# Kernel tuning notes

Measured on AMD Instinct MI355X. Metric: run time of the kernel, lower is better.

The kernel has to match this reference:

```python
import jax, jax.numpy as jnp
import numpy as np
from jax import lax

CR = 16        # opt.cr (temporal dim)
HEADS = 4      # num_heads
DIM = 64       # dim == channel count c
B = 2          # true batch; input batch = B*CR
H = W = 128


def setup_inputs() -> dict:
    key = jax.random.key(0)
    k1, k2, k3, k4 = jax.random.split(key, 4)
    return {
        "x": jax.random.normal(k1, (B * CR, DIM, H, W), jnp.float32),
        "ln_weight": jnp.ones((DIM,), jnp.float32),
        "ln_bias": jnp.zeros((DIM,), jnp.float32),
        "qkv_w": jax.random.normal(k2, (3 * CR, CR), jnp.float32) * 0.05,   # 1x1 conv
        "dw_w": jax.random.normal(k3, (3 * CR, 1, 3, 3), jnp.float32) * 0.1,  # depthwise 3x3
        "proj_w": jax.random.normal(k4, (DIM, DIM), jnp.float32) * 0.05,   # 1x1 conv
        "temperature": jnp.ones((HEADS, 1, 1), jnp.float32),
    }


def reference(x, ln_weight, ln_bias, qkv_w, dw_w, proj_w, temperature):
    b, c, h, w = x.shape
    Bt = b // CR
    # WithBias LayerNorm over channel dim (per spatial location), eps=1e-5
    mu = jnp.mean(x, axis=1, keepdims=True)
    var = jnp.mean(jnp.square(x - mu), axis=1, keepdims=True)
    xn = (x - mu) / jnp.sqrt(var + 1e-5)
    xn = xn * ln_weight[None, :, None, None] + ln_bias[None, :, None, None]
    # (B*cr, c, h, w) -> (B, cr, c, h, w) -> (B*c, cr, h, w)
    x_in = xn.reshape(Bt, CR, c, h, w).transpose(0, 2, 1, 3, 4).reshape(Bt * c, CR, h, w)
    # 1x1 qkv conv (no bias)
    qkv = jnp.einsum('oc,bchw->bohw', qkv_w, x_in)
    # depthwise 3x3 conv, padding 1
    qkv = lax.conv_general_dilated(qkv, dw_w, (1, 1), 'SAME',
                                   feature_group_count=3 * CR,
                                   dimension_numbers=('NCHW', 'OIHW', 'NCHW'))
    q, k, v = jnp.split(qkv, 3, axis=1)
    ch = CR // HEADS  # per-head channel dim

    def heads(t):
        return t.reshape(Bt * c, HEADS, ch, h * w)

    def l2n(t):
        n = jnp.sqrt(jnp.sum(jnp.square(t), axis=-1, keepdims=True))
        return t / jnp.maximum(n, 1e-12)

    q, k, v = heads(q), heads(k), heads(v)
    q, k = l2n(q), l2n(k)
    # transposed (channel) attention: small ch x ch scores
    attn = jnp.einsum('bhcn,bhdn->bhcd', q, k) * temperature[None]
    attn = jax.nn.softmax(attn, axis=-1)
    out = jnp.einsum('bhcd,bhdn->bhcn', attn, v)  # (B*c, heads, ch, hw)
    # (B*c, cr, h, w) -> (B, c, cr, h, w) -> (B*cr, c, h, w)
    out = out.reshape(Bt * c, CR, h, w).reshape(Bt, c, CR, h, w)
    out = out.transpose(0, 2, 1, 3, 4).reshape(b, c, h, w)
    # 1x1 project_out
    return jnp.einsum('oc,bchw->bohw', proj_w, out)
```

## Files before the change

kernel.cpp:

```cpp
#include <hip/hip_runtime.h>
#include <hip/hip_fp16.h>

typedef _Float16 half8_t __attribute__((ext_vector_type(8)));
typedef float float4_t __attribute__((ext_vector_type(4)));

__device__ __forceinline__ float2 h2f2(unsigned int u) {
  return __half22float2(__builtin_bit_cast(__half2, u));
}
__device__ __forceinline__ unsigned int f2h2(float a, float b) {
  return __builtin_bit_cast(unsigned int, __floats2half2_rn(a, b));
}

#if __has_builtin(__builtin_amdgcn_fdot2)
typedef _Float16 h2v __attribute__((ext_vector_type(2)));
__device__ __forceinline__ float fdot2(unsigned int a, unsigned int b, float c) {
  return __builtin_amdgcn_fdot2(__builtin_bit_cast(h2v, a),
                                __builtin_bit_cast(h2v, b), c, false);
}
#else
__device__ __forceinline__ float fdot2(unsigned int a, unsigned int b, float c) {
  float2 fa = h2f2(a), fb = h2f2(b);
  return fmaf(fa.y, fb.y, fmaf(fa.x, fb.x, c));
}
#endif

__global__ __launch_bounds__(256) void k_stats(const float2* __restrict__ x2,
                                               float4* __restrict__ stats4) {
  int id = blockIdx.x * 256 + threadIdx.x;
  int bb = id >> 13;
  int jp = id & 8191;
  const float2* xp = x2 + ((size_t)bb << 19) + jp;
  float s0 = 0.f, q0 = 0.f, s1 = 0.f, q1 = 0.f;
#pragma unroll
  for (int ci = 0; ci < 64; ++ci) {
    float2 v = xp[(size_t)ci << 13];
    s0 += v.x; q0 = fmaf(v.x, v.x, q0);
    s1 += v.y; q1 = fmaf(v.y, v.y, q1);
  }
  float mu0 = s0 * (1.f / 64.f), mu1 = s1 * (1.f / 64.f);
  float4 r;
  r.x = mu0; r.y = rsqrtf(fmaf(-mu0, mu0, q0 * (1.f / 64.f)) + 1e-5f);
  r.z = mu1; r.w = rsqrtf(fmaf(-mu1, mu1, q1 * (1.f / 64.f)) + 1e-5f);
  stats4[id] = r;
}

__global__ __launch_bounds__(256) void k_wpack(
    const float* __restrict__ qkvw, const float* __restrict__ dww,
    const float* __restrict__ projw, unsigned int* __restrict__ qkvpk,
    unsigned int* __restrict__ dwpk, unsigned int* __restrict__ projpk) {
  int t = blockIdx.x * 256 + threadIdx.x;
  if (t < 2048) {
    int o = t >> 5, c2 = t & 31;
    projpk[t] = f2h2(projw[(o << 6) + 2 * c2], projw[(o << 6) + 2 * c2 + 1]);
  } else if (t < 2432) {
    int i = t - 2048;
    int ch = i >> 3, tp = i & 7;
    qkvpk[i] = f2h2(qkvw[(ch << 4) + 2 * tp], qkvw[(ch << 4) + 2 * tp + 1]);
  } else if (t < 2648) {
    int i = t - 2432;
    int pl = i / 9, k = i - pl * 9;
    dwpk[i] = f2h2(dww[18 * pl + k], dww[18 * pl + 9 + k]);
  }
}

__global__ __launch_bounds__(256) void k_fused(
    const float* __restrict__ x, const float2* __restrict__ stats2,
    const float* __restrict__ lnw, const float* __restrict__ lnb,
    const unsigned int* __restrict__ qkvpk, const unsigned int* __restrict__ dwpk,
    unsigned int* __restrict__ vbuf, float* __restrict__ Sacc,
    float* __restrict__ Nacc) {
  __shared__ unsigned int xnl[2944];
  __shared__ unsigned int pre[2976];
  __shared__ unsigned int qk[2080];
  int tid = threadIdx.x;
  int bc = blockIdx.y, bt = bc >> 6, ci = bc & 63;
  int tx0 = (blockIdx.x & 3) << 5;
  int ty0 = (blockIdx.x >> 2) << 3;
  float lw = lnw[ci], lb = lnb[ci];

  {
    size_t xci = ((size_t)(bt * 1024 + ci)) << 14;
    int sb = bt << 18;
#pragma unroll
    for (int it = 0; it < 2; ++it) {
      int pos = tid + (it << 8);
      if (pos < 360) {
        int hy = pos / 36, hx = pos - hy * 36;
        int gy = ty0 + hy - 1, gx = tx0 + hx - 1;
        bool ok = (hx < 34) && ((unsigned)gy < 128u) && ((unsigned)gx < 128u);
        int gp = (gy << 7) + gx;
        unsigned int w[8];
#pragma unroll
        for (int tp = 0; tp < 8; ++tp) {
          unsigned int ww = 0;
          if (ok) {
            float x0 = x[xci + ((size_t)(2 * tp) << 20) + gp];
            float x1 = x[xci + ((size_t)(2 * tp + 1) << 20) + gp];
            float2 s0 = stats2[sb + ((2 * tp) << 14) + gp];
            float2 s1 = stats2[sb + ((2 * tp + 1) << 14) + gp];
            ww = f2h2(fmaf((x0 - s0.x) * s0.y, lw, lb),
                      fmaf((x1 - s1.x) * s1.y, lw, lb));
          }
          w[tp] = ww;
        }
        *reinterpret_cast<uint4*>(&xnl[pos * 4]) = make_uint4(w[0], w[1], w[2], w[3]);
        *reinterpret_cast<uint4*>(&xnl[1472 + pos * 4]) =
            make_uint4(w[4], w[5], w[6], w[7]);
      }
    }
  }
  __syncthreads();

  int lane15 = tid & 15;
  int kg = (tid >> 4) & 3;
  int wv = tid >> 6;
  int jx = tid & 7, iy = (tid >> 3) & 7, pq = wv;

  for (int m = 0; m < 3; ++m) {
    if (m > 0) {
      int pm = m - 1;
      {
        int combo = tid >> 3, pc = tid & 7;
        int hp_ = combo >> 4, cd = combo & 15, cc = cd >> 2, dd = cd & 3;
        const unsigned int* qrow = qk + (4 * hp_ + cc) * 130;
        const unsigned int* krow = qk + (8 + 4 * hp_ + dd) * 130;
        float s = 0.f;
#pragma unroll
        for (int i = 0; i < 8; ++i) {
          uint2 q2 = *reinterpret_cast<const uint2*>(&qrow[2 * pc + (i << 4)]);
          uint2 k2 = *reinterpret_cast<const uint2*>(&krow[2 * pc + (i << 4)]);
          s = fdot2(q2.x, k2.x, s);
          s = fdot2(q2.y, k2.y, s);
        }
        s += __shfl_xor(s, 1); s += __shfl_xor(s, 2); s += __shfl_xor(s, 4);
        if (pc == 0)
          atomicAdd(&Sacc[((bc << 2) + 2 * pm + hp_) * 16 + cc * 4 + dd], s);
      }
      {
        int row = tid >> 4, pc = tid & 15;
        const unsigned int* rp = qk + row * 130;
        float n = 0.f;
#pragma unroll
        for (int i = 0; i < 4; ++i) {
          uint2 v2 = *reinterpret_cast<const uint2*>(&rp[2 * pc + (i << 5)]);
          n = fdot2(v2.x, v2.x, n);
          n = fdot2(v2.y, v2.y, n);
        }
        n += __shfl_xor(n, 1); n += __shfl_xor(n, 2);
        n += __shfl_xor(n, 4); n += __shfl_xor(n, 8);
        if (pc == 0) {
          int g = (row < 8) ? (8 * pm + row) : (16 + 8 * pm + (row - 8));
          atomicAdd(&Nacc[(bc << 5) + g], n);
        }
      }
    }
    {
      int gch = (m < 2)
                    ? ((lane15 < 8) ? (8 * m + lane15) : (16 + 8 * m + (lane15 - 8)))
                    : (32 + lane15);
      uint4 aw = make_uint4(0, 0, 0, 0);
      if (kg < 2) aw = *reinterpret_cast<const uint4*>(&qkvpk[gch * 8 + 4 * kg]);
      half8_t af = __builtin_bit_cast(half8_t, aw);
      float4_t zz = {0.f, 0.f, 0.f, 0.f};
      for (int T = wv; T < 23; T += 4) {
        int hp = T * 16 + lane15;
        uint4 bw = make_uint4(0, 0, 0, 0);
        if (kg < 2)
          bw = *reinterpret_cast<const uint4*>(&xnl[kg * 1472 + hp * 4]);
        half8_t bf = __builtin_bit_cast(half8_t, bw);
        float4_t d = __builtin_amdgcn_mfma_f32_16x16x32_f16(af, bf, zz, 0, 0, 0);
        pre[(2 * kg) * 372 + hp] = f2h2(d[0], d[1]);
        pre[(2 * kg + 1) * 372 + hp] = f2h2(d[2], d[3]);
      }
    }
    __syncthreads();
#pragma unroll
    for (int p2 = 0; p2 < 2; ++p2) {
      int pl = pq + 4 * p2;
      int gpl = (m < 2) ? ((pl < 4) ? (4 * m + pl) : (8 + 4 * m + (pl - 4)))
                        : (16 + pl);
      const unsigned int* wp = dwpk + gpl * 9;
      __half2 a0 = __floats2half2_rn(0.f, 0.f), a1 = a0, a2 = a0, a3 = a0;
      int base = pl * 372 + iy * 36 + 4 * jx;
#pragma unroll
      for (int dy = 0; dy < 3; ++dy) {
        uint4 C0 = *reinterpret_cast<const uint4*>(&pre[base + dy * 36]);
        uint2 C1 = *reinterpret_cast<const uint2*>(&pre[base + dy * 36 + 4]);
        __half2 c0 = __builtin_bit_cast(__half2, C0.x);
        __half2 c1 = __builtin_bit_cast(__half2, C0.y);
        __half2 c2 = __builtin_bit_cast(__half2, C0.z);
        __half2 c3 = __builtin_bit_cast(__half2, C0.w);
        __half2 c4 = __builtin_bit_cast(__half2, C1.x);
        __half2 c5 = __builtin_bit_cast(__half2, C1.y);
        __half2 w0 = __builtin_bit_cast(__half2, wp[dy * 3 + 0]);
        __half2 w1 = __builtin_bit_cast(__half2, wp[dy * 3 + 1]);
        __half2 w2 = __builtin_bit_cast(__half2, wp[dy * 3 + 2]);
        a0 = __hfma2(w0, c0, a0); a0 = __hfma2(w1, c1, a0); a0 = __hfma2(w2, c2, a0);
        a1 = __hfma2(w0, c1, a1); a1 = __hfma2(w1, c2, a1); a1 = __hfma2(w2, c3, a1);
        a2 = __hfma2(w0, c2, a2); a2 = __hfma2(w1, c3, a2); a2 = __hfma2(w2, c4, a2);
        a3 = __hfma2(w0, c3, a3); a3 = __hfma2(w1, c4, a3); a3 = __hfma2(w2, c5, a3);
      }
      unsigned int u0 = __builtin_bit_cast(unsigned int, a0);
      unsigned int u1 = __builtin_bit_cast(unsigned int, a1);
      unsigned int u2 = __builtin_bit_cast(unsigned int, a2);
      unsigned int u3 = __builtin_bit_cast(unsigned int, a3);
      if (m < 2) {
        uint2 E, O;
        E.x = (u0 & 0xFFFFu) | (u1 << 16);
        E.y = (u2 & 0xFFFFu) | (u3 << 16);
        O.x = (u0 >> 16) | (u1 & 0xFFFF0000u);
        O.y = (u2 >> 16) | (u3 & 0xFFFF0000u);
        int pp = iy * 16 + 2 * jx;
        *reinterpret_cast<uint2*>(&qk[(2 * pl) * 130 + pp]) = E;
        *reinterpret_cast<uint2*>(&qk[(2 * pl + 1) * 130 + pp]) = O;
      } else {
        size_t idx = ((size_t)(bc * 8 + pl) << 14) +
                     (size_t)((ty0 + iy) << 7) + tx0 + 4 * jx;
        *reinterpret_cast<uint4*>(&vbuf[idx]) = make_uint4(u0, u1, u2, u3);
      }
    }
    if (m < 2) __syncthreads();
  }
}

__global__ __launch_bounds__(256) void k_softmax(
    const float* __restrict__ Sacc, const float* __restrict__ Nacc,
    const float* __restrict__ temp, unsigned int* __restrict__ attnpk) {
  int idx = blockIdx.x * 256 + threadIdx.x;
  if (idx >= 512) return;
  int b = idx >> 2, hd = idx & 3;
  int bt = b >> 6, ci = b & 63;
  float tp = temp[hd];
  float iq[4], ik[4];
#pragma unroll
  for (int c = 0; c < 4; ++c) {
    iq[c] = 1.f / fmaxf(sqrtf(Nacc[(b << 5) + (hd << 2) + c]), 1e-12f);
    ik[c] = 1.f / fmaxf(sqrtf(Nacc[(b << 5) + 16 + (hd << 2) + c]), 1e-12f);
  }
  const float* Sp = Sacc + ((b << 2) + hd) * 16;
#pragma unroll
  for (int c = 0; c < 4; ++c) {
    float l[4];
#pragma unroll
    for (int d = 0; d < 4; ++d) l[d] = Sp[c * 4 + d] * iq[c] * ik[d] * tp;
    float m = fmaxf(fmaxf(l[0], l[1]), fmaxf(l[2], l[3]));
    float e0 = expf(l[0] - m), e1 = expf(l[1] - m);
    float e2 = expf(l[2] - m), e3 = expf(l[3] - m);
    float inv = 1.f / (e0 + e1 + e2 + e3);
    unsigned int* dst = attnpk + ((((bt * 4 + hd) * 4 + c) << 7) + ci * 2);
    dst[0] = f2h2(e0 * inv, e1 * inv);
    dst[1] = f2h2(e2 * inv, e3 * inv);
  }
}

__global__ __launch_bounds__(256) void k_outproj(
    const unsigned int* __restrict__ vbuf, const unsigned int* __restrict__ attnpk,
    const unsigned int* __restrict__ projpk, float* __restrict__ out) {
  __shared__ unsigned int Yl[32 * 260];
  __shared__ unsigned int attn_l[128];
  int tid = threadIdx.x;
  int comb = blockIdx.y;
  int bt = comb >> 4, hd = (comb >> 2) & 3;
  int lane15 = tid & 15;
  int kg = (tid >> 4) & 3;
  int wv = tid >> 6;

  if (tid < 128)
    attn_l[tid] = attnpk[((((bt << 2) + hd) * 4 + (comb & 3)) << 7) + tid];
  __syncthreads();

  {
    int gpx = (blockIdx.x << 8) + tid;
    size_t vb = (((size_t)bt * 512 + hd * 2) << 14) + gpx;
#pragma unroll
    for (int ci2 = 0; ci2 < 32; ++ci2) {
      size_t b0 = vb + (((size_t)(2 * ci2) * 8) << 14);
      size_t b1 = b0 + ((size_t)8 << 14);
      unsigned int va0 = vbuf[b0], vb0 = vbuf[b0 + 16384];
      unsigned int va1 = vbuf[b1], vb1 = vbuf[b1 + 16384];
      uint4 aw = *reinterpret_cast<const uint4*>(&attn_l[4 * ci2]);
      float y0 = fdot2(va0, aw.x, fdot2(vb0, aw.y, 0.f));
      float y1 = fdot2(va1, aw.z, fdot2(vb1, aw.w, 0.f));
      Yl[ci2 * 260 + tid] = f2h2(y0, y1);
    }
  }
  __syncthreads();

  half8_t A0[4], A1[4];
#pragma unroll
  for (int ot = 0; ot < 4; ++ot) {
    A0[ot] = __builtin_bit_cast(
        half8_t, *reinterpret_cast<const uint4*>(
                     &projpk[(ot * 16 + lane15) * 32 + kg * 4]));
    A1[ot] = __builtin_bit_cast(
        half8_t, *reinterpret_cast<const uint4*>(
                     &projpk[(ot * 16 + lane15) * 32 + 16 + kg * 4]));
  }
  float4_t zz = {0.f, 0.f, 0.f, 0.f};
  size_t outbase = ((size_t)comb << 20) + (blockIdx.x << 8);
#pragma unroll
  for (int pt = 0; pt < 4; ++pt) {
    int pxl = wv * 64 + pt * 16 + lane15;
    unsigned int r0 = Yl[(kg * 4 + 0) * 260 + pxl];
    unsigned int r1 = Yl[(kg * 4 + 1) * 260 + pxl];
    unsigned int r2 = Yl[(kg * 4 + 2) * 260 + pxl];
    unsigned int r3 = Yl[(kg * 4 + 3) * 260 + pxl];
    half8_t B0 = __builtin_bit_cast(half8_t, make_uint4(r0, r1, r2, r3));
    unsigned int s0 = Yl[(16 + kg * 4 + 0) * 260 + pxl];
    unsigned int s1 = Yl[(16 + kg * 4 + 1) * 260 + pxl];
    unsigned int s2 = Yl[(16 + kg * 4 + 2) * 260 + pxl];
    unsigned int s3 = Yl[(16 + kg * 4 + 3) * 260 + pxl];
    half8_t B1 = __builtin_bit_cast(half8_t, make_uint4(s0, s1, s2, s3));
#pragma unroll
    for (int ot = 0; ot < 4; ++ot) {
      float4_t d = __builtin_amdgcn_mfma_f32_16x16x32_f16(A0[ot], B0, zz, 0, 0, 0);
      d = __builtin_amdgcn_mfma_f32_16x16x32_f16(A1[ot], B1, d, 0, 0, 0);
      int o0 = ot * 16 + kg * 4;
#pragma unroll
      for (int r = 0; r < 4; ++r)
        out[outbase + ((size_t)(o0 + r) << 14) + pxl] = d[r];
    }
  }
}

extern "C" void kernel_launch(void* const* d_in, const int* in_sizes, int n_in,
                              void* d_out, int out_size, void* d_ws, size_t ws_size,
                              hipStream_t stream) {
  const float* x = (const float*)d_in[0];
  const float* lnw = (const float*)d_in[1];
  const float* lnb = (const float*)d_in[2];
  const float* qkvw = (const float*)d_in[3];
  const float* dww = (const float*)d_in[4];
  const float* projw = (const float*)d_in[5];
  const float* temp = (const float*)d_in[6];
  float* out = (float*)d_out;

  unsigned int* vbuf = (unsigned int*)d_ws;
  char* tail = (char*)d_ws + 67108864ull;
  float4* stats4 = (float4*)tail;
  float* Sacc = (float*)(tail + 4194304ull);
  float* Nacc = Sacc + 8192;
  unsigned int* attnpk = (unsigned int*)(Nacc + 4096);
  unsigned int* projpk = attnpk + 4096;
  unsigned int* qkvpk = projpk + 2048;
  unsigned int* dwpk = qkvpk + 384;

  hipMemsetAsync(Sacc, 0, (8192 + 4096) * sizeof(float), stream);
  k_stats<<<dim3(1024), dim3(256), 0, stream>>>((const float2*)x, stats4);
  k_wpack<<<dim3(11), dim3(256), 0, stream>>>(qkvw, dww, projw, qkvpk, dwpk, projpk);
  k_fused<<<dim3(64, 128), dim3(256), 0, stream>>>(
      x, (const float2*)stats4, lnw, lnb, qkvpk, dwpk, vbuf, Sacc, Nacc);
  k_softmax<<<dim3(2), dim3(256), 0, stream>>>(Sacc, Nacc, temp, attnpk);
  k_outproj<<<dim3(64, 32), dim3(256), 0, stream>>>(vbuf, attnpk, projpk, out);
}
```

Before: 214.9 us.

## Fuse weight packing and softmax into neighbours, vectorize halo loads

Weight packing moves into an extra block of the stats kernel, and the tiny softmax kernel is folded into the prologue of the output-projection kernel, which removes two launches. The fused kernel's halo load now has each thread handle two adjacent pixels, using float2 x loads and float4 stats loads, with a shifted halo origin (tx0-2) so the 8-byte loads stay aligned. The depthwise conv reads shift by one to match the new halo layout. The cost is that softmax is recomputed redundantly in every output-projection block, and the halo load uses fewer threads.

```diff
diff --git a/kernel.cpp b/kernel.cpp
--- a/kernel.cpp
+++ b/kernel.cpp
@@ -24,8 +24,28 @@
 }
 #endif
 
-__global__ __launch_bounds__(256) void k_stats(const float2* __restrict__ x2,
-                                               float4* __restrict__ stats4) {
+__global__ __launch_bounds__(256) void k_stats(
+    const float2* __restrict__ x2, float4* __restrict__ stats4,
+    const float* __restrict__ qkvw, const float* __restrict__ dww,
+    const float* __restrict__ projw, unsigned int* __restrict__ qkvpk,
+    unsigned int* __restrict__ dwpk, unsigned int* __restrict__ projpk) {
+  if (blockIdx.x >= 1024) {
+    for (int t = threadIdx.x; t < 2648; t += 256) {
+      if (t < 2048) {
+        int o = t >> 5, c2 = t & 31;
+        projpk[t] = f2h2(projw[(o << 6) + 2 * c2], projw[(o << 6) + 2 * c2 + 1]);
+      } else if (t < 2432) {
+        int i = t - 2048;
+        int ch = i >> 3, tp = i & 7;
+        qkvpk[i] = f2h2(qkvw[(ch << 4) + 2 * tp], qkvw[(ch << 4) + 2 * tp + 1]);
+      } else {
+        int i = t - 2432;
+        int pl = i / 9, k = i - pl * 9;
+        dwpk[i] = f2h2(dww[18 * pl + k], dww[18 * pl + 9 + k]);
+      }
+    }
+    return;
+  }
   int id = blockIdx.x * 256 + threadIdx.x;
   int bb = id >> 13;
   int jp = id & 8191;
@@ -44,27 +64,8 @@
   stats4[id] = r;
 }
 
-__global__ __launch_bounds__(256) void k_wpack(
-    const float* __restrict__ qkvw, const float* __restrict__ dww,
-    const float* __restrict__ projw, unsigned int* __restrict__ qkvpk,
-    unsigned int* __restrict__ dwpk, unsigned int* __restrict__ projpk) {
-  int t = blockIdx.x * 256 + threadIdx.x;
-  if (t < 2048) {
-    int o = t >> 5, c2 = t & 31;
-    projpk[t] = f2h2(projw[(o << 6) + 2 * c2], projw[(o << 6) + 2 * c2 + 1]);
-  } else if (t < 2432) {
-    int i = t - 2048;
-    int ch = i >> 3, tp = i & 7;
-    qkvpk[i] = f2h2(qkvw[(ch << 4) + 2 * tp], qkvw[(ch << 4) + 2 * tp + 1]);
-  } else if (t < 2648) {
-    int i = t - 2432;
-    int pl = i / 9, k = i - pl * 9;
-    dwpk[i] = f2h2(dww[18 * pl + k], dww[18 * pl + 9 + k]);
-  }
-}
-
 __global__ __launch_bounds__(256) void k_fused(
-    const float* __restrict__ x, const float2* __restrict__ stats2,
+    const float* __restrict__ x, const float4* __restrict__ stats4,
     const float* __restrict__ lnw, const float* __restrict__ lnb,
     const unsigned int* __restrict__ qkvpk, const unsigned int* __restrict__ dwpk,
     unsigned int* __restrict__ vbuf, float* __restrict__ Sacc,
@@ -78,36 +79,37 @@
   int ty0 = (blockIdx.x >> 2) << 3;
   float lw = lnw[ci], lb = lnb[ci];
 
-  {
-    size_t xci = ((size_t)(bt * 1024 + ci)) << 14;
-    int sb = bt << 18;
-#pragma unroll
-    for (int it = 0; it < 2; ++it) {
-      int pos = tid + (it << 8);
-      if (pos < 360) {
-        int hy = pos / 36, hx = pos - hy * 36;
-        int gy = ty0 + hy - 1, gx = tx0 + hx - 1;
-        bool ok = (hx < 34) && ((unsigned)gy < 128u) && ((unsigned)gx < 128u);
-        int gp = (gy << 7) + gx;
-        unsigned int w[8];
-#pragma unroll
-        for (int tp = 0; tp < 8; ++tp) {
-          unsigned int ww = 0;
-          if (ok) {
-            float x0 = x[xci + ((size_t)(2 * tp) << 20) + gp];
-            float x1 = x[xci + ((size_t)(2 * tp + 1) << 20) + gp];
-            float2 s0 = stats2[sb + ((2 * tp) << 14) + gp];
-            float2 s1 = stats2[sb + ((2 * tp + 1) << 14) + gp];
-            ww = f2h2(fmaf((x0 - s0.x) * s0.y, lw, lb),
-                      fmaf((x1 - s1.x) * s1.y, lw, lb));
-          }
-          w[tp] = ww;
-        }
-        *reinterpret_cast<uint4*>(&xnl[pos * 4]) = make_uint4(w[0], w[1], w[2], w[3]);
-        *reinterpret_cast<uint4*>(&xnl[1472 + pos * 4]) =
-            make_uint4(w[4], w[5], w[6], w[7]);
-      }
-    }
+  if (tid < 180) {
+    int hy = tid / 18, hpx = tid - hy * 18;
+    int gy = ty0 + hy - 1;
+    int gx = tx0 - 2 + 2 * hpx;
+    bool ok = ((unsigned)gy < 128u) && ((unsigned)gx < 127u);
+    unsigned int w0[8], w1[8];
+#pragma unroll
+    for (int tp = 0; tp < 8; ++tp) { w0[tp] = 0; w1[tp] = 0; }
+    if (ok) {
+      size_t xci = ((size_t)(bt * 1024 + ci) << 14) + (gy << 7) + gx;
+      int jp = (gy << 6) + (gx >> 1);
+#pragma unroll
+      for (int tp = 0; tp < 8; ++tp) {
+        float2 xa = *reinterpret_cast<const float2*>(&x[xci + ((size_t)(2 * tp) << 20)]);
+        float2 xb = *reinterpret_cast<const float2*>(&x[xci + ((size_t)(2 * tp + 1) << 20)]);
+        float4 sa = stats4[((size_t)((bt << 4) + 2 * tp) << 13) + jp];
+        float4 sb = stats4[((size_t)((bt << 4) + 2 * tp + 1) << 13) + jp];
+        w0[tp] = f2h2(fmaf((xa.x - sa.x) * sa.y, lw, lb),
+                      fmaf((xb.x - sb.x) * sb.y, lw, lb));
+        w1[tp] = f2h2(fmaf((xa.y - sa.z) * sa.w, lw, lb),
+                      fmaf((xb.y - sb.z) * sb.w, lw, lb));
+      }
+    }
+    int pos = hy * 36 + 2 * hpx;
+    *reinterpret_cast<uint4*>(&xnl[pos * 4]) = make_uint4(w0[0], w0[1], w0[2], w0[3]);
+    *reinterpret_cast<uint4*>(&xnl[(pos + 1) * 4]) =
+        make_uint4(w1[0], w1[1], w1[2], w1[3]);
+    *reinterpret_cast<uint4*>(&xnl[1472 + pos * 4]) =
+        make_uint4(w0[4], w0[5], w0[6], w0[7]);
+    *reinterpret_cast<uint4*>(&xnl[1472 + (pos + 1) * 4]) =
+        make_uint4(w1[4], w1[5], w1[6], w1[7]);
   }
   __syncthreads();
 
@@ -185,20 +187,20 @@
 #pragma unroll
       for (int dy = 0; dy < 3; ++dy) {
         uint4 C0 = *reinterpret_cast<const uint4*>(&pre[base + dy * 36]);
-        uint2 C1 = *reinterpret_cast<const uint2*>(&pre[base + dy * 36 + 4]);
-        __half2 c0 = __builtin_bit_cast(__half2, C0.x);
+        uint4 C1 = *reinterpret_cast<const uint4*>(&pre[base + dy * 36 + 4]);
         __half2 c1 = __builtin_bit_cast(__half2, C0.y);
         __half2 c2 = __builtin_bit_cast(__half2, C0.z);
         __half2 c3 = __builtin_bit_cast(__half2, C0.w);
         __half2 c4 = __builtin_bit_cast(__half2, C1.x);
         __half2 c5 = __builtin_bit_cast(__half2, C1.y);
+        __half2 c6 = __builtin_bit_cast(__half2, C1.z);
         __half2 w0 = __builtin_bit_cast(__half2, wp[dy * 3 + 0]);
         __half2 w1 = __builtin_bit_cast(__half2, wp[dy * 3 + 1]);
         __half2 w2 = __builtin_bit_cast(__half2, wp[dy * 3 + 2]);
-        a0 = __hfma2(w0, c0, a0); a0 = __hfma2(w1, c1, a0); a0 = __hfma2(w2, c2, a0);
-        a1 = __hfma2(w0, c1, a1); a1 = __hfma2(w1, c2, a1); a1 = __hfma2(w2, c3, a1);
-        a2 = __hfma2(w0, c2, a2); a2 = __hfma2(w1, c3, a2); a2 = __hfma2(w2, c4, a2);
-        a3 = __hfma2(w0, c3, a3); a3 = __hfma2(w1, c4, a3); a3 = __hfma2(w2, c5, a3);
+        a0 = __hfma2(w0, c1, a0); a0 = __hfma2(w1, c2, a0); a0 = __hfma2(w2, c3, a0);
+        a1 = __hfma2(w0, c2, a1); a1 = __hfma2(w1, c3, a1); a1 = __hfma2(w2, c4, a1);
+        a2 = __hfma2(w0, c3, a2); a2 = __hfma2(w1, c4, a2); a2 = __hfma2(w2, c5, a2);
+        a3 = __hfma2(w0, c4, a3); a3 = __hfma2(w1, c5, a3); a3 = __hfma2(w2, c6, a3);
       }
       unsigned int u0 = __builtin_bit_cast(unsigned int, a0);
       unsigned int u1 = __builtin_bit_cast(unsigned int, a1);
@@ -223,50 +225,36 @@
   }
 }
 
-__global__ __launch_bounds__(256) void k_softmax(
-    const float* __restrict__ Sacc, const float* __restrict__ Nacc,
-    const float* __restrict__ temp, unsigned int* __restrict__ attnpk) {
-  int idx = blockIdx.x * 256 + threadIdx.x;
-  if (idx >= 512) return;
-  int b = idx >> 2, hd = idx & 3;
-  int bt = b >> 6, ci = b & 63;
-  float tp = temp[hd];
-  float iq[4], ik[4];
-#pragma unroll
-  for (int c = 0; c < 4; ++c) {
-    iq[c] = 1.f / fmaxf(sqrtf(Nacc[(b << 5) + (hd << 2) + c]), 1e-12f);
-    ik[c] = 1.f / fmaxf(sqrtf(Nacc[(b << 5) + 16 + (hd << 2) + c]), 1e-12f);
-  }
-  const float* Sp = Sacc + ((b << 2) + hd) * 16;
-#pragma unroll
-  for (int c = 0; c < 4; ++c) {
-    float l[4];
-#pragma unroll
-    for (int d = 0; d < 4; ++d) l[d] = Sp[c * 4 + d] * iq[c] * ik[d] * tp;
-    float m = fmaxf(fmaxf(l[0], l[1]), fmaxf(l[2], l[3]));
-    float e0 = expf(l[0] - m), e1 = expf(l[1] - m);
-    float e2 = expf(l[2] - m), e3 = expf(l[3] - m);
-    float inv = 1.f / (e0 + e1 + e2 + e3);
-    unsigned int* dst = attnpk + ((((bt * 4 + hd) * 4 + c) << 7) + ci * 2);
-    dst[0] = f2h2(e0 * inv, e1 * inv);
-    dst[1] = f2h2(e2 * inv, e3 * inv);
-  }
-}
-
 __global__ __launch_bounds__(256) void k_outproj(
-    const unsigned int* __restrict__ vbuf, const unsigned int* __restrict__ attnpk,
+    const unsigned int* __restrict__ vbuf, const float* __restrict__ Sacc,
+    const float* __restrict__ Nacc, const float* __restrict__ temp,
     const unsigned int* __restrict__ projpk, float* __restrict__ out) {
   __shared__ unsigned int Yl[32 * 260];
   __shared__ unsigned int attn_l[128];
   int tid = threadIdx.x;
   int comb = blockIdx.y;
-  int bt = comb >> 4, hd = (comb >> 2) & 3;
+  int bt = comb >> 4, hd = (comb >> 2) & 3, c = comb & 3;
   int lane15 = tid & 15;
   int kg = (tid >> 4) & 3;
   int wv = tid >> 6;
 
-  if (tid < 128)
-    attn_l[tid] = attnpk[((((bt << 2) + hd) * 4 + (comb & 3)) << 7) + tid];
+  if (tid < 64) {
+    int b = (bt << 6) + tid;
+    float tp = temp[hd];
+    float iq = 1.f / fmaxf(sqrtf(Nacc[(b << 5) + (hd << 2) + c]), 1e-12f);
+    float l[4];
+#pragma unroll
+    for (int d = 0; d < 4; ++d) {
+      float ik = 1.f / fmaxf(sqrtf(Nacc[(b << 5) + 16 + (hd << 2) + d]), 1e-12f);
+      l[d] = Sacc[((b << 2) + hd) * 16 + c * 4 + d] * iq * ik * tp;
+    }
+    float mx = fmaxf(fmaxf(l[0], l[1]), fmaxf(l[2], l[3]));
+    float e0 = expf(l[0] - mx), e1 = expf(l[1] - mx);
+    float e2 = expf(l[2] - mx), e3 = expf(l[3] - mx);
+    float inv = 1.f / (e0 + e1 + e2 + e3);
+    attn_l[2 * tid] = f2h2(e0 * inv, e1 * inv);
+    attn_l[2 * tid + 1] = f2h2(e2 * inv, e3 * inv);
+  }
   __syncthreads();
 
   {
@@ -340,16 +328,15 @@
   float4* stats4 = (float4*)tail;
   float* Sacc = (float*)(tail + 4194304ull);
   float* Nacc = Sacc + 8192;
-  unsigned int* attnpk = (unsigned int*)(Nacc + 4096);
-  unsigned int* projpk = attnpk + 4096;
+  unsigned int* projpk = (unsigned int*)(Nacc + 4096);
   unsigned int* qkvpk = projpk + 2048;
   unsigned int* dwpk = qkvpk + 384;
 
   hipMemsetAsync(Sacc, 0, (8192 + 4096) * sizeof(float), stream);
-  k_stats<<<dim3(1024), dim3(256), 0, stream>>>((const float2*)x, stats4);
-  k_wpack<<<dim3(11), dim3(256), 0, stream>>>(qkvw, dww, projw, qkvpk, dwpk, projpk);
+  k_stats<<<dim3(1025), dim3(256), 0, stream>>>((const float2*)x, stats4, qkvw,
+                                                dww, projw, qkvpk, dwpk, projpk);
   k_fused<<<dim3(64, 128), dim3(256), 0, stream>>>(
-      x, (const float2*)stats4, lnw, lnb, qkvpk, dwpk, vbuf, Sacc, Nacc);
-  k_softmax<<<dim3(2), dim3(256), 0, stream>>>(Sacc, Nacc, temp, attnpk);
-  k_outproj<<<dim3(64, 32), dim3(256), 0, stream>>>(vbuf, attnpk, projpk, out);
-}
+      x, stats4, lnw, lnb, qkvpk, dwpk, vbuf, Sacc, Nacc);
+  k_outproj<<<dim3(64, 32), dim3(256), 0, stream>>>(vbuf, Sacc, Nacc, temp,
+                                                    projpk, out);
+}
```

Result: faster. 200.7 us (-6.6%).
